# Kernel optimization log

Measured on AMD Instinct MI355X. Metric: run time of the kernel, lower is better.

Reference implementation:

```python
import jax, jax.numpy as jnp
import numpy as np

B, S, IN = 8, 1024, 64
D, F, H, L = 512, 2048, 8, 6
HD = D // H
EPS = 1e-5
GATE_TEMP = 1.0


def _rmsnorm(x, scale):
    return x * scale * jax.lax.rsqrt(jnp.mean(x * x, axis=-1, keepdims=True) + EPS)


def _sinusoidal_pe(seq_len, d_model):
    pos = np.arange(seq_len)[:, None].astype(np.float32)
    div = np.exp(np.arange(0, d_model, 2).astype(np.float32) * (-np.log(10000.0) / d_model))
    pe = np.zeros((seq_len, d_model), dtype=np.float32)
    pe[:, 0::2] = np.sin(pos * div)
    pe[:, 1::2] = np.cos(pos * div)
    return jnp.asarray(pe)


def setup_inputs() -> dict:
    key = jax.random.key(0)
    ks = jax.random.split(key, 12)
    s = 0.02
    return {
        "src": jax.random.normal(ks[0], (B, S, IN), jnp.float32),
        "in_w": jax.random.normal(ks[1], (IN, D), jnp.float32) * s,
        "in_b": jnp.zeros((D,), jnp.float32),
        "Wq": jax.random.normal(ks[2], (L, D, D), jnp.float32) * s,
        "Wk": jax.random.normal(ks[3], (L, D, D), jnp.float32) * s,
        "Wv": jax.random.normal(ks[4], (L, D, D), jnp.float32) * s,
        "Wo": jax.random.normal(ks[5], (L, D, D), jnp.float32) * s,
        "bq": jnp.zeros((L, D), jnp.float32),
        "bk": jnp.zeros((L, D), jnp.float32),
        "bv": jnp.zeros((L, D), jnp.float32),
        "bo": jnp.zeros((L, D), jnp.float32),
        "n1": jnp.ones((L, D), jnp.float32),
        "n2": jnp.ones((L, D), jnp.float32),
        "Wg": jax.random.normal(ks[6], (L, D, F), jnp.float32) * s,
        "Wu": jax.random.normal(ks[7], (L, D, F), jnp.float32) * s,
        "Wd": jax.random.normal(ks[8], (L, F, D), jnp.float32) * s,
        "gate_w": jax.random.normal(ks[9], (L, D), jnp.float32) * s,
        "gate_b": jnp.full((L,), 2.0, jnp.float32),  # LayerGate init_bias=2.0
        "final_scale": jnp.ones((D,), jnp.float32),
    }


def reference(src, in_w, in_b, Wq, Wk, Wv, Wo, bq, bk, bv, bo, n1, n2,
              Wg, Wu, Wd, gate_w, gate_b, final_scale):
    b, s, _ = src.shape
    x = src @ in_w + in_b                      # input_adapter: [B,S,D]
    x = x + _sinusoidal_pe(s, D)               # PositionalEncoding, scale=1.0
    inv_sqrt_hd = 1.0 / jnp.sqrt(jnp.asarray(HD, x.dtype))
    for i in range(L):
        # --- pre-norm self-attention block ---
        h = _rmsnorm(x, n1[i])
        q = (h @ Wq[i] + bq[i]).reshape(b, s, H, HD)
        k = (h @ Wk[i] + bk[i]).reshape(b, s, H, HD)
        v = (h @ Wv[i] + bv[i]).reshape(b, s, H, HD)
        scores = jnp.einsum("bqhd,bkhd->bhqk", q, k) * inv_sqrt_hd
        attn = jax.nn.softmax(scores, axis=-1)
        ctx = jnp.einsum("bhqk,bkhd->bqhd", attn, v).reshape(b, s, D)
        y = x + (ctx @ Wo[i] + bo[i])
        # --- pre-norm SwiGLU FFN block ---
        h2 = _rmsnorm(y, n2[i])
        y = y + (jax.nn.silu(h2 @ Wg[i]) * (h2 @ Wu[i])) @ Wd[i]
        # --- LayerGate: seq-mode hard skip with straight-through estimator ---
        pooled = jnp.mean(x, axis=1)                           # gate on layer input [B,D]
        p = jax.nn.sigmoid((pooled @ gate_w[i] + gate_b[i]) / GATE_TEMP)  # [B]
        hard = (p > 0.5).astype(x.dtype)
        g = hard + p - jax.lax.stop_gradient(p)
        x = g[:, None, None] * y + (1.0 - g)[:, None, None] * x
    return _rmsnorm(x, final_scale)
```

## Files before the change

### kernel.cpp

```cpp
#include <hip/hip_runtime.h>


typedef unsigned short u16;
typedef __attribute__((ext_vector_type(8))) __bf16 bf16x8;
typedef __attribute__((ext_vector_type(4))) float f32x4;
typedef __attribute__((ext_vector_type(16))) float f32x16;
typedef __attribute__((ext_vector_type(8))) unsigned short u16x8;

#define DEV __device__ __forceinline__

DEV u16 f2bf(float f) {
  unsigned u = __builtin_bit_cast(unsigned, f);
  u += 0x7fffu + ((u >> 16) & 1u);
  return (u16)(u >> 16);
}
DEV float bf2f(u16 h) { return __builtin_bit_cast(float, ((unsigned)h) << 16); }

DEV void gload16(const void* g, void* l) {
  __builtin_amdgcn_global_load_lds(
      (__attribute__((address_space(1))) void*)g,
      (__attribute__((address_space(3))) void*)l, 16, 0, 0);
}

DEV void xcd_map(int& bx, int& by) {
  const int nx = gridDim.x, ny = gridDim.y;
  const int orig = bx * ny + by;
  const int cpx = (nx * ny) >> 3;
  const int swz = (orig & 7) * cpx + (orig >> 3);
  bx = swz / ny; by = swz - bx * ny;
}

__global__ __launch_bounds__(256) void transpose_all_kernel(
    const float* __restrict__ Wq, const float* __restrict__ Wk,
    const float* __restrict__ Wv, const float* __restrict__ Wo,
    const float* __restrict__ Wg, const float* __restrict__ Wu,
    const float* __restrict__ Wd,
    u16* __restrict__ WqkvT, u16* __restrict__ WoT, u16* __restrict__ WgT,
    u16* __restrict__ WuT, u16* __restrict__ WdT)
{
  const int l = blockIdx.y;
  const int idx = blockIdx.x;
  const float* src; u16* dst; int N, bx, by;
  if (idx < 1024) {
    const int w = idx >> 8, t = idx & 255;
    bx = t & 15; by = t >> 4; N = 512;
    const size_t lo = (size_t)l * 262144;
    if (w == 0)      { src = Wq + lo; dst = WqkvT + (size_t)l * 786432; }
    else if (w == 1) { src = Wk + lo; dst = WqkvT + (size_t)l * 786432 + 262144; }
    else if (w == 2) { src = Wv + lo; dst = WqkvT + (size_t)l * 786432 + 524288; }
    else             { src = Wo + lo; dst = WoT + lo; }
  } else if (idx < 2048) {
    const int t = idx - 1024; bx = t & 63; by = t >> 6; N = 2048;
    src = Wg + (size_t)l * 1048576; dst = WgT + (size_t)l * 1048576;
  } else if (idx < 3072) {
    const int t = idx - 2048; bx = t & 63; by = t >> 6; N = 2048;
    src = Wu + (size_t)l * 1048576; dst = WuT + (size_t)l * 1048576;
  } else {
    const int t = idx - 3072; bx = t & 15; by = t >> 4; N = 512;
    src = Wd + (size_t)l * 1048576; dst = WdT + (size_t)l * 1048576;
  }
  const int K = (idx >= 3072) ? 2048 : 512;
  __shared__ float tl[32][33];
  const int n0 = bx * 32, k0 = by * 32;
  const int tx = threadIdx.x & 31, ty = threadIdx.x >> 5;
#pragma unroll
  for (int i = 0; i < 4; ++i)
    tl[ty + i * 8][tx] = src[(size_t)(k0 + ty + i * 8) * N + n0 + tx];
  __syncthreads();
#pragma unroll
  for (int i = 0; i < 4; ++i)
    dst[(size_t)(n0 + ty + i * 8) * K + k0 + tx] = f2bf(tl[tx][ty + i * 8]);
}

__global__ void biaspack_kernel(const float* __restrict__ bq,
                                const float* __restrict__ bk,
                                const float* __restrict__ bv,
                                float* __restrict__ out)
{
  const int l = blockIdx.x;
  for (int c = threadIdx.x; c < 1536; c += 256) {
    float v = (c < 512) ? bq[l * 512 + c]
            : (c < 1024) ? bk[l * 512 + c - 512]
                         : bv[l * 512 + c - 1024];
    out[l * 1536 + c] = v;
  }
}

__global__ __launch_bounds__(256) void adapter_kernel(
    const float* __restrict__ src, const float* __restrict__ w,
    const float* __restrict__ bias, float* __restrict__ x)
{
  __shared__ float srow[8][64];
  const int m0 = blockIdx.y * 8;
  const int n = blockIdx.x * 256 + threadIdx.x;
  for (int i = threadIdx.x; i < 512; i += 256)
    srow[i >> 6][i & 63] = src[(size_t)m0 * 64 + i];
  __syncthreads();
  float acc[8];
#pragma unroll
  for (int r = 0; r < 8; ++r) acc[r] = bias[n];
  for (int k = 0; k < 64; ++k) {
    const float wv = w[(size_t)k * 512 + n];
#pragma unroll
    for (int r = 0; r < 8; ++r) acc[r] = fmaf(srow[r][k], wv, acc[r]);
  }
  const int i2 = n & ~1;
  const float freq = expf((float)i2 * (-9.210340371976184f / 512.0f));
#pragma unroll
  for (int r = 0; r < 8; ++r) {
    const int pos = (m0 + r) & 1023;
    const float ang = (float)pos * freq;
    acc[r] += (n & 1) ? cosf(ang) : sinf(ang);
    x[(size_t)(m0 + r) * 512 + n] = acc[r];
  }
}

template <bool BF16OUT>
__global__ __launch_bounds__(256) void rmsnorm_kernel(
    const float* __restrict__ x, const float* __restrict__ scale,
    u16* __restrict__ outb, float* __restrict__ outf)
{
  const int wave = threadIdx.x >> 6, lane = threadIdx.x & 63;
  const size_t row = (size_t)blockIdx.x * 4 + wave;
  const f32x4* xr = (const f32x4*)(x + row * 512);
  f32x4 a = xr[lane * 2], c = xr[lane * 2 + 1];
  float ss = a[0]*a[0] + a[1]*a[1] + a[2]*a[2] + a[3]*a[3]
           + c[0]*c[0] + c[1]*c[1] + c[2]*c[2] + c[3]*c[3];
#pragma unroll
  for (int d = 1; d < 64; d <<= 1) ss += __shfl_xor(ss, d);
  const float r = rsqrtf(ss * (1.0f / 512.0f) + 1e-5f);
  const f32x4* sr = (const f32x4*)scale;
  f32x4 s1 = sr[lane * 2], s2 = sr[lane * 2 + 1];
  if (BF16OUT) {
    u16x8 ov;
    ov[0] = f2bf(a[0] * s1[0] * r); ov[1] = f2bf(a[1] * s1[1] * r);
    ov[2] = f2bf(a[2] * s1[2] * r); ov[3] = f2bf(a[3] * s1[3] * r);
    ov[4] = f2bf(c[0] * s2[0] * r); ov[5] = f2bf(c[1] * s2[1] * r);
    ov[6] = f2bf(c[2] * s2[2] * r); ov[7] = f2bf(c[3] * s2[3] * r);
    *(u16x8*)(outb + row * 512 + lane * 8) = ov;
  } else {
    f32x4 o1, o2;
    o1[0] = a[0]*s1[0]*r; o1[1] = a[1]*s1[1]*r; o1[2] = a[2]*s1[2]*r; o1[3] = a[3]*s1[3]*r;
    o2[0] = c[0]*s2[0]*r; o2[1] = c[1]*s2[1]*r; o2[2] = c[2]*s2[2]*r; o2[3] = c[3]*s2[3]*r;
    f32x4* orow = (f32x4*)(outf + row * 512);
    orow[lane * 2] = o1; orow[lane * 2 + 1] = o2;
  }
}

template <int MODE, int BN>
__global__ __launch_bounds__(256) void gemm_bt(
    const u16* __restrict__ A, const u16* __restrict__ Bt,
    const float* __restrict__ bias, const float* __restrict__ resf,
    float* __restrict__ outf, u16* __restrict__ outb,
    const float* __restrict__ gatep, int M, int N, int K)
{
  constexpr int NI = BN / 32;
  constexpr int BROUNDS = BN / 64;
  __shared__ __align__(16) u16 lA[128 * 32];
  __shared__ __align__(16) u16 lB[BN * 32];
  const int tid = threadIdx.x;
  const int wave = tid >> 6, lane = tid & 63;
  const int lr = lane & 15, lg = lane >> 4;
  int bx = blockIdx.x, by = blockIdx.y;
  xcd_map(bx, by);
  const int m0 = by << 7, n0 = bx * BN;
  const int wr = wave >> 1, wc = wave & 1;
  if (MODE == 4) {
    if (gatep[m0 >> 10] == 0.0f) return;
  }
  f32x4 acc[4][NI] = {};
  for (int kt = 0; kt < K; kt += 32) {
    __syncthreads();
#pragma unroll
    for (int i = 0; i < 2; ++i) {
      const int c = i * 256 + tid;
      const int row = c >> 2, kc = (c & 3) << 3;
      gload16(A + (size_t)(m0 + row) * K + kt + kc,
              lA + (size_t)(i * 256 + wave * 64) * 8);
    }
#pragma unroll
    for (int i = 0; i < BROUNDS; ++i) {
      const int c = i * 256 + tid;
      const int row = c >> 2, kc = (c & 3) << 3;
      gload16(Bt + (size_t)(n0 + row) * K + kt + kc,
              lB + (size_t)(i * 256 + wave * 64) * 8);
    }
    __syncthreads();
    bf16x8 af[4], bfr[NI];
#pragma unroll
    for (int mi = 0; mi < 4; ++mi)
      af[mi] = *(const bf16x8*)&lA[(wr * 64 + mi * 16 + lr) * 32 + lg * 8];
#pragma unroll
    for (int ni = 0; ni < NI; ++ni)
      bfr[ni] = *(const bf16x8*)&lB[(wc * (BN / 2) + ni * 16 + lr) * 32 + lg * 8];
#pragma unroll
    for (int mi = 0; mi < 4; ++mi)
#pragma unroll
      for (int ni = 0; ni < NI; ++ni)
        acc[mi][ni] = __builtin_amdgcn_mfma_f32_16x16x32_bf16(
            af[mi], bfr[ni], acc[mi][ni], 0, 0, 0);
  }
#pragma unroll
  for (int mi = 0; mi < 4; ++mi) {
#pragma unroll
    for (int ni = 0; ni < NI; ++ni) {
      const int col = n0 + wc * (BN / 2) + ni * 16 + lr;
      const float bs = (MODE == 0 || MODE == 1) ? bias[col] : 0.0f;
#pragma unroll
      for (int j = 0; j < 4; ++j) {
        const int row = m0 + wr * 64 + mi * 16 + lg * 4 + j;
        const size_t idx = (size_t)row * N + col;
        float v = acc[mi][ni][j] + bs;
        if (MODE == 0) {
          if (col < 512) v *= 0.125f;
          outb[idx] = f2bf(v);
        } else {
          outf[idx] = v + resf[idx];
        }
      }
    }
  }
}

__global__ __launch_bounds__(256) void gemm_glu(
    const u16* __restrict__ A, const u16* __restrict__ Bg,
    const u16* __restrict__ Bu, u16* __restrict__ outT)
{
  constexpr int K = 512, N = 2048;
  __shared__ __align__(16) u16 lA[128 * 32];
  __shared__ __align__(16) u16 lG[64 * 32];
  __shared__ __align__(16) u16 lU[64 * 32];
  const int tid = threadIdx.x;
  const int wave = tid >> 6, lane = tid & 63;
  const int lr = lane & 15, lg = lane >> 4;
  int bx = blockIdx.x, by = blockIdx.y;
  xcd_map(bx, by);
  const int m0 = by << 7, n0 = bx << 6;
  const int wr = wave >> 1, wc = wave & 1;
  f32x4 ag[4][2] = {}, au[4][2] = {};
  for (int kt = 0; kt < K; kt += 32) {
    __syncthreads();
#pragma unroll
    for (int i = 0; i < 2; ++i) {
      const int c = i * 256 + tid;
      const int row = c >> 2, kc = (c & 3) << 3;
      gload16(A + (size_t)(m0 + row) * K + kt + kc,
              lA + (size_t)(i * 256 + wave * 64) * 8);
    }
    {
      const int row = tid >> 2, kc = (tid & 3) << 3;
      gload16(Bg + (size_t)(n0 + row) * K + kt + kc, lG + (size_t)(wave * 64) * 8);
      gload16(Bu + (size_t)(n0 + row) * K + kt + kc, lU + (size_t)(wave * 64) * 8);
    }
    __syncthreads();
    bf16x8 af[4], gf[2], uf[2];
#pragma unroll
    for (int mi = 0; mi < 4; ++mi)
      af[mi] = *(const bf16x8*)&lA[(wr * 64 + mi * 16 + lr) * 32 + lg * 8];
#pragma unroll
    for (int ni = 0; ni < 2; ++ni) {
      gf[ni] = *(const bf16x8*)&lG[(wc * 32 + ni * 16 + lr) * 32 + lg * 8];
      uf[ni] = *(const bf16x8*)&lU[(wc * 32 + ni * 16 + lr) * 32 + lg * 8];
    }
#pragma unroll
    for (int mi = 0; mi < 4; ++mi)
#pragma unroll
      for (int ni = 0; ni < 2; ++ni) {
        ag[mi][ni] = __builtin_amdgcn_mfma_f32_16x16x32_bf16(
            af[mi], gf[ni], ag[mi][ni], 0, 0, 0);
        au[mi][ni] = __builtin_amdgcn_mfma_f32_16x16x32_bf16(
            af[mi], uf[ni], au[mi][ni], 0, 0, 0);
      }
  }
#pragma unroll
  for (int mi = 0; mi < 4; ++mi) {
#pragma unroll
    for (int ni = 0; ni < 2; ++ni) {
      const int col = n0 + wc * 32 + ni * 16 + lr;
#pragma unroll
      for (int j = 0; j < 4; ++j) {
        const int row = m0 + wr * 64 + mi * 16 + lg * 4 + j;
        const float g = ag[mi][ni][j];
        const float sg = g / (1.0f + __expf(-g));
        outT[(size_t)row * N + col] = f2bf(sg * au[mi][ni][j]);
      }
    }
  }
}

__global__ __launch_bounds__(256) void attn_kernel(
    const u16* __restrict__ qkv, u16* __restrict__ ctx)
{
  constexpr int LD = 1536;
  const int qblk = blockIdx.x, bh = blockIdx.y;
  const int b = bh >> 3, h = bh & 7;
  const int tid = threadIdx.x, wave = tid >> 6, lane = tid & 63;
  const int l31 = lane & 31, half = lane >> 5;
  const size_t rowb = (size_t)b * 1024;
  const int q0 = qblk * 128 + wave * 32;

  __shared__ __align__(16) u16 Ksh[2][64 * 64];
  __shared__ __align__(16) u16 Vsh[2][64 * 64];
  __shared__ __align__(16) u16 PL[4][32 * 64];
  __shared__ float rl_lds[4][32];

  const u16* qrow = qkv + (rowb + q0 + l31) * LD + h * 64;
  bf16x8 qf[4];
#pragma unroll
  for (int c = 0; c < 4; ++c)
    qf[c] = *(const bf16x8*)(qrow + c * 16 + half * 8);

  const int krow0 = tid >> 3;
  const int kch0 = (tid & 7) ^ (krow0 & 7);
  const int kch1 = (tid & 7) ^ ((krow0 + 32) & 7);
  const int vm = tid >> 3, vd0 = (tid & 7) * 8;
  const int vswz = (vm >> 2) ^ (tid & 7);
  char* vbase0 = (char*)Vsh + (vswz << 4) + ((vm & 3) << 2);
  const u16* kg = qkv + rowb * LD + 512 + h * 64;
  const u16* vg = qkv + (rowb + 2 * vm) * LD + 1024 + h * 64 + vd0;

  f32x16 o0 = {}, o1 = {};
  float l_acc = 0.0f;

  gload16(kg + (size_t)(0 + krow0) * LD + kch0 * 8, Ksh[0] + wave * 512);
  gload16(kg + (size_t)(32 + krow0) * LD + kch1 * 8, Ksh[0] + 2048 + wave * 512);
  {
    u16x8 va = *(const u16x8*)vg;
    u16x8 vb = *(const u16x8*)(vg + LD);
#pragma unroll
    for (int j = 0; j < 8; ++j) {
      const unsigned w = (unsigned)va[j] | ((unsigned)vb[j] << 16);
      *(unsigned*)(vbase0 + (vd0 + j) * 128) = w;
    }
  }
  __syncthreads();

  for (int t = 0; t < 16; ++t) {
    const int cur = t & 1, nxt = cur ^ 1;
    const int k0n = (t + 1) * 64;
    u16x8 va2, vb2;
    if (t < 15) {
      gload16(kg + (size_t)(k0n + krow0) * LD + kch0 * 8,
              Ksh[nxt] + wave * 512);
      gload16(kg + (size_t)(k0n + 32 + krow0) * LD + kch1 * 8,
              Ksh[nxt] + 2048 + wave * 512);
      va2 = *(const u16x8*)(vg + (size_t)k0n * LD);
      vb2 = *(const u16x8*)(vg + (size_t)k0n * LD + LD);
    }

    const char* kshb = (const char*)Ksh[cur];
    const char* vshb = (const char*)Vsh[cur];

    f32x16 s0 = {}, s1 = {};
#pragma unroll
    for (int c = 0; c < 4; ++c) {
      {
        const int row = l31;
        bf16x8 kf = *(const bf16x8*)(kshb + row * 128 +
                        ((((c << 1) | half) ^ (row & 7)) << 4));
        s0 = __builtin_amdgcn_mfma_f32_32x32x16_bf16(kf, qf[c], s0, 0, 0, 0);
      }
      {
        const int row = 32 + l31;
        bf16x8 kf = *(const bf16x8*)(kshb + row * 128 +
                        ((((c << 1) | half) ^ (row & 7)) << 4));
        s1 = __builtin_amdgcn_mfma_f32_32x32x16_bf16(kf, qf[c], s1, 0, 0, 0);
      }
    }

    char* plw = (char*)PL[wave];
#pragma unroll
    for (int blk = 0; blk < 2; ++blk) {
      const f32x16 sv = blk ? s1 : s0;
#pragma unroll
      for (int rg = 0; rg < 4; ++rg) {
        const float e0 = __expf(fminf(sv[rg * 4 + 0], 60.0f));
        const float e1 = __expf(fminf(sv[rg * 4 + 1], 60.0f));
        const float e2 = __expf(fminf(sv[rg * 4 + 2], 60.0f));
        const float e3 = __expf(fminf(sv[rg * 4 + 3], 60.0f));
        l_acc += (e0 + e1) + (e2 + e3);
        const unsigned lo = (unsigned)f2bf(e0) | ((unsigned)f2bf(e1) << 16);
        const unsigned hi = (unsigned)f2bf(e2) | ((unsigned)f2bf(e3) << 16);
        const int chunk = (rg + 4 * blk) ^ (l31 & 7);
        *(unsigned long long*)(plw + l31 * 128 + (chunk << 4) + half * 8) =
            (unsigned long long)lo | ((unsigned long long)hi << 32);
      }
    }

#pragma unroll
    for (int c = 0; c < 4; ++c) {
      bf16x8 pf = *(const bf16x8*)(plw + l31 * 128 +
                      ((((c << 1) | half) ^ (l31 & 7)) << 4));
      {
        const int row = l31;
        bf16x8 vf = *(const bf16x8*)(vshb + row * 128 +
                        ((((c << 1) | half) ^ (row >> 3)) << 4));
        o0 = __builtin_amdgcn_mfma_f32_32x32x16_bf16(pf, vf, o0, 0, 0, 0);
      }
      {
        const int row = 32 + l31;
        bf16x8 vf = *(const bf16x8*)(vshb + row * 128 +
                        ((((c << 1) | half) ^ (row >> 3)) << 4));
        o1 = __builtin_amdgcn_mfma_f32_32x32x16_bf16(pf, vf, o1, 0, 0, 0);
      }
    }

    if (t < 15) {
      char* vbn = (char*)Vsh[nxt] + (vswz << 4) + ((vm & 3) << 2);
#pragma unroll
      for (int j = 0; j < 8; ++j) {
        const unsigned w = (unsigned)va2[j] | ((unsigned)vb2[j] << 16);
        *(unsigned*)(vbn + (vd0 + j) * 128) = w;
      }
    }
    __syncthreads();
  }

  const float l_tot = l_acc + __shfl_xor(l_acc, 32);
  if (lane < 32) rl_lds[wave][l31] = 1.0f / l_tot;
  __syncthreads();
#pragma unroll
  for (int r = 0; r < 16; ++r) {
    const int q_r = (r & 3) + 8 * (r >> 2) + 4 * half;
    const float rl = rl_lds[wave][q_r];
    const size_t orow = (rowb + q0 + q_r) * 512 + h * 64 + l31;
    ctx[orow] = f2bf(o0[r] * rl);
    ctx[orow + 32] = f2bf(o1[r] * rl);
  }
}

__global__ __launch_bounds__(256) void gate_partial_kernel(
    const float* __restrict__ x, const float* __restrict__ gw,
    float* __restrict__ gp)
{
  const int b = blockIdx.x, chunk = blockIdx.y, tid = threadIdx.x;
  const float* xb = x + (size_t)b * 1024 * 512 + (size_t)chunk * 16 * 512;
  float acc = 0.0f;
#pragma unroll
  for (int k = 0; k < 8; ++k) {
    const int i = tid * 4 + k * 1024;
    f32x4 v = *(const f32x4*)(xb + i);
    f32x4 wv = *(const f32x4*)(gw + (i & 511));
    acc += v[0]*wv[0] + v[1]*wv[1] + v[2]*wv[2] + v[3]*wv[3];
  }
  __shared__ float red[256];
  red[tid] = acc;
  __syncthreads();
  for (int s = 128; s > 32; s >>= 1) {
    if (tid < s) red[tid] += red[tid + s];
    __syncthreads();
  }
  if (tid < 32) {
    float v = red[tid] + red[tid + 32];
#pragma unroll
    for (int d = 1; d < 32; d <<= 1) v += __shfl_xor(v, d);
    if (tid == 0) gp[b * 64 + chunk] = v;
  }
}

__global__ __launch_bounds__(512) void gate_final_kernel(
    const float* __restrict__ gp, const float* __restrict__ gb, int layer,
    float* __restrict__ gout)
{
  const int tid = threadIdx.x, b = tid >> 6, lane = tid & 63;
  float v = gp[tid];
#pragma unroll
  for (int d = 1; d < 64; d <<= 1) v += __shfl_xor(v, d);
  if (lane == 0) {
    const float val = v / 1024.0f + gb[layer];
    const float p = 1.0f / (1.0f + __expf(-val));
    gout[b] = (p > 0.5f) ? 1.0f : 0.0f;
  }
}

extern "C" void kernel_launch(void* const* d_in, const int* in_sizes, int n_in,
                              void* d_out, int out_size, void* d_ws, size_t ws_size,
                              hipStream_t stream)
{
  (void)in_sizes; (void)n_in; (void)out_size; (void)ws_size;
  const float* src  = (const float*)d_in[0];
  const float* in_w = (const float*)d_in[1];
  const float* in_b = (const float*)d_in[2];
  const float* Wq   = (const float*)d_in[3];
  const float* Wk   = (const float*)d_in[4];
  const float* Wv   = (const float*)d_in[5];
  const float* Wo   = (const float*)d_in[6];
  const float* bq   = (const float*)d_in[7];
  const float* bk   = (const float*)d_in[8];
  const float* bv   = (const float*)d_in[9];
  const float* bo   = (const float*)d_in[10];
  const float* n1   = (const float*)d_in[11];
  const float* n2   = (const float*)d_in[12];
  const float* Wg   = (const float*)d_in[13];
  const float* Wu   = (const float*)d_in[14];
  const float* Wd   = (const float*)d_in[15];
  const float* gw   = (const float*)d_in[16];
  const float* gb   = (const float*)d_in[17];
  const float* fs   = (const float*)d_in[18];

  char* ws = (char*)d_ws;
  size_t off = 0;
  auto alloc = [&](size_t bytes) -> void* {
    void* p = ws + off;
    off += (bytes + 255) & ~(size_t)255;
    return p;
  };
  u16*   WqkvT = (u16*)alloc(6ULL * 1536 * 512 * 2);
  u16*   WoT   = (u16*)alloc(6ULL * 512 * 512 * 2);
  u16*   WgT   = (u16*)alloc(6ULL * 2048 * 512 * 2);
  u16*   WuT   = (u16*)alloc(6ULL * 2048 * 512 * 2);
  u16*   WdT   = (u16*)alloc(6ULL * 512 * 2048 * 2);
  float* bqkv  = (float*)alloc(6ULL * 1536 * 4);
  float* x     = (float*)alloc(8192ULL * 512 * 4);
  float* y     = (float*)alloc(8192ULL * 512 * 4);
  u16*   hbuf  = (u16*)alloc(8192ULL * 512 * 2);
  u16*   sA    = (u16*)alloc(8192ULL * 2048 * 2);
  u16*   sB    = (u16*)alloc(8192ULL * 2048 * 2);
  float* gp    = (float*)alloc(512 * 4);
  float* gate  = (float*)alloc(64 * 4);

  const dim3 tb(256);
  transpose_all_kernel<<<dim3(4096, 6), tb, 0, stream>>>(
      Wq, Wk, Wv, Wo, Wg, Wu, Wd, WqkvT, WoT, WgT, WuT, WdT);
  biaspack_kernel<<<6, tb, 0, stream>>>(bq, bk, bv, bqkv);
  adapter_kernel<<<dim3(2, 1024), tb, 0, stream>>>(src, in_w, in_b, x);

  for (int l = 0; l < 6; ++l) {
    gate_partial_kernel<<<dim3(8, 64), tb, 0, stream>>>(x, gw + l * 512, gp);
    gate_final_kernel<<<1, 512, 0, stream>>>(gp, gb, l, gate);
    rmsnorm_kernel<true><<<2048, tb, 0, stream>>>(x, n1 + l * 512, hbuf, nullptr);
    gemm_bt<0, 128><<<dim3(12, 64), tb, 0, stream>>>(
        hbuf, WqkvT + (size_t)l * 1536 * 512, bqkv + l * 1536,
        nullptr, nullptr, sA, nullptr, 8192, 1536, 512);
    attn_kernel<<<dim3(8, 64), tb, 0, stream>>>(sA, sB);
    gemm_bt<1, 64><<<dim3(8, 64), tb, 0, stream>>>(
        sB, WoT + (size_t)l * 512 * 512, bo + l * 512,
        x, y, nullptr, nullptr, 8192, 512, 512);
    rmsnorm_kernel<true><<<2048, tb, 0, stream>>>(y, n2 + l * 512, hbuf, nullptr);
    gemm_glu<<<dim3(32, 64), tb, 0, stream>>>(
        hbuf, WgT + (size_t)l * 2048 * 512, WuT + (size_t)l * 2048 * 512, sB);
    gemm_bt<4, 64><<<dim3(8, 64), tb, 0, stream>>>(
        sB, WdT + (size_t)l * 512 * 2048, nullptr,
        y, x, nullptr, gate, 8192, 512, 2048);
  }
  rmsnorm_kernel<false><<<2048, tb, 0, stream>>>(x, fs, nullptr, (float*)d_out);
}
```

Baseline: 1.128 ms.

## Double GEMM K-tile with XOR-swizzled LDS, fold gate final into down GEMM

The GEMM kernels now stage 64-wide K tiles instead of 32, with an XOR swizzle on the LDS layout. This halves the barrier and loop iterations and should cut LDS bank conflicts. The separate gate_final launch is removed, and each down-projection block reduces the gate partials itself and compares against zero instead of applying a sigmoid. The XCD block mapping switches to row-major order, and the attention kernel's second K-chunk swizzle index is simplified. LDS use per block roughly doubles, which may lower occupancy.

```diff
diff --git a/kernel.cpp b/kernel.cpp
--- a/kernel.cpp
+++ b/kernel.cpp
@@ -24,10 +24,10 @@
 
 DEV void xcd_map(int& bx, int& by) {
   const int nx = gridDim.x, ny = gridDim.y;
-  const int orig = bx * ny + by;
+  const int orig = by * nx + bx;
   const int cpx = (nx * ny) >> 3;
   const int swz = (orig & 7) * cpx + (orig >> 3);
-  bx = swz / ny; by = swz - bx * ny;
+  by = swz / nx; bx = swz - by * nx;
 }
 
 __global__ __launch_bounds__(256) void transpose_all_kernel(
@@ -152,12 +152,12 @@
     const u16* __restrict__ A, const u16* __restrict__ Bt,
     const float* __restrict__ bias, const float* __restrict__ resf,
     float* __restrict__ outf, u16* __restrict__ outb,
-    const float* __restrict__ gatep, int M, int N, int K)
+    const float* __restrict__ gatep, const float* __restrict__ gbias,
+    int layer, int M, int N, int K)
 {
   constexpr int NI = BN / 32;
-  constexpr int BROUNDS = BN / 64;
-  __shared__ __align__(16) u16 lA[128 * 32];
-  __shared__ __align__(16) u16 lB[BN * 32];
+  __shared__ __align__(16) u16 lA[128 * 64];
+  __shared__ __align__(16) u16 lB[BN * 64];
   const int tid = threadIdx.x;
   const int wave = tid >> 6, lane = tid & 63;
   const int lr = lane & 15, lg = lane >> 4;
@@ -166,39 +166,56 @@
   const int m0 = by << 7, n0 = bx * BN;
   const int wr = wave >> 1, wc = wave & 1;
   if (MODE == 4) {
-    if (gatep[m0 >> 10] == 0.0f) return;
+    __shared__ float gfl;
+    if (tid < 64) {
+      float v = gatep[(m0 >> 10) * 64 + tid];
+#pragma unroll
+      for (int d = 1; d < 64; d <<= 1) v += __shfl_xor(v, d);
+      if (tid == 0) gfl = (v / 1024.0f + gbias[layer] > 0.0f) ? 1.0f : 0.0f;
+    }
+    __syncthreads();
+    if (gfl == 0.0f) return;
   }
   f32x4 acc[4][NI] = {};
-  for (int kt = 0; kt < K; kt += 32) {
-    __syncthreads();
-#pragma unroll
-    for (int i = 0; i < 2; ++i) {
+  for (int kt = 0; kt < K; kt += 64) {
+    __syncthreads();
+#pragma unroll
+    for (int i = 0; i < 4; ++i) {
       const int c = i * 256 + tid;
-      const int row = c >> 2, kc = (c & 3) << 3;
+      const int row = c >> 3, kc = ((c & 7) ^ (row & 7)) << 3;
       gload16(A + (size_t)(m0 + row) * K + kt + kc,
               lA + (size_t)(i * 256 + wave * 64) * 8);
     }
 #pragma unroll
-    for (int i = 0; i < BROUNDS; ++i) {
+    for (int i = 0; i < BN / 32; ++i) {
       const int c = i * 256 + tid;
-      const int row = c >> 2, kc = (c & 3) << 3;
+      const int row = c >> 3, kc = ((c & 7) ^ (row & 7)) << 3;
       gload16(Bt + (size_t)(n0 + row) * K + kt + kc,
               lB + (size_t)(i * 256 + wave * 64) * 8);
     }
     __syncthreads();
-    bf16x8 af[4], bfr[NI];
-#pragma unroll
-    for (int mi = 0; mi < 4; ++mi)
-      af[mi] = *(const bf16x8*)&lA[(wr * 64 + mi * 16 + lr) * 32 + lg * 8];
-#pragma unroll
-    for (int ni = 0; ni < NI; ++ni)
-      bfr[ni] = *(const bf16x8*)&lB[(wc * (BN / 2) + ni * 16 + lr) * 32 + lg * 8];
-#pragma unroll
-    for (int mi = 0; mi < 4; ++mi)
-#pragma unroll
-      for (int ni = 0; ni < NI; ++ni)
-        acc[mi][ni] = __builtin_amdgcn_mfma_f32_16x16x32_bf16(
-            af[mi], bfr[ni], acc[mi][ni], 0, 0, 0);
+    bf16x8 af[2][4], bfr[2][NI];
+#pragma unroll
+    for (int kk = 0; kk < 2; ++kk) {
+#pragma unroll
+      for (int mi = 0; mi < 4; ++mi) {
+        const int row = wr * 64 + mi * 16 + lr;
+        af[kk][mi] = *(const bf16x8*)&lA[row * 64 + (((kk * 4 + lg) ^ (row & 7)) << 3)];
+      }
+#pragma unroll
+      for (int ni = 0; ni < NI; ++ni) {
+        const int row = wc * (BN / 2) + ni * 16 + lr;
+        bfr[kk][ni] = *(const bf16x8*)&lB[row * 64 + (((kk * 4 + lg) ^ (row & 7)) << 3)];
+      }
+    }
+#pragma unroll
+    for (int kk = 0; kk < 2; ++kk)
+#pragma unroll
+      for (int mi = 0; mi < 4; ++mi)
+#pragma unroll
+        for (int ni = 0; ni < NI; ++ni)
+          acc[mi][ni] = __builtin_amdgcn_mfma_f32_16x16x32_bf16(
+              af[kk][mi], bfr[kk][ni], acc[mi][ni], 0, 0, 0);
   }
 #pragma unroll
   for (int mi = 0; mi < 4; ++mi) {
@@ -227,9 +244,9 @@
     const u16* __restrict__ Bu, u16* __restrict__ outT)
 {
   constexpr int K = 512, N = 2048;
-  __shared__ __align__(16) u16 lA[128 * 32];
-  __shared__ __align__(16) u16 lG[64 * 32];
-  __shared__ __align__(16) u16 lU[64 * 32];
+  __shared__ __align__(16) u16 lA[128 * 64];
+  __shared__ __align__(16) u16 lG[64 * 64];
+  __shared__ __align__(16) u16 lU[64 * 64];
   const int tid = threadIdx.x;
   const int wave = tid >> 6, lane = tid & 63;
   const int lr = lane & 15, lg = lane >> 4;
@@ -238,39 +255,51 @@
   const int m0 = by << 7, n0 = bx << 6;
   const int wr = wave >> 1, wc = wave & 1;
   f32x4 ag[4][2] = {}, au[4][2] = {};
-  for (int kt = 0; kt < K; kt += 32) {
-    __syncthreads();
+  for (int kt = 0; kt < K; kt += 64) {
+    __syncthreads();
+#pragma unroll
+    for (int i = 0; i < 4; ++i) {
+      const int c = i * 256 + tid;
+      const int row = c >> 3, kc = ((c & 7) ^ (row & 7)) << 3;
+      gload16(A + (size_t)(m0 + row) * K + kt + kc,
+              lA + (size_t)(i * 256 + wave * 64) * 8);
+    }
 #pragma unroll
     for (int i = 0; i < 2; ++i) {
       const int c = i * 256 + tid;
-      const int row = c >> 2, kc = (c & 3) << 3;
-      gload16(A + (size_t)(m0 + row) * K + kt + kc,
-              lA + (size_t)(i * 256 + wave * 64) * 8);
-    }
-    {
-      const int row = tid >> 2, kc = (tid & 3) << 3;
-      gload16(Bg + (size_t)(n0 + row) * K + kt + kc, lG + (size_t)(wave * 64) * 8);
-      gload16(Bu + (size_t)(n0 + row) * K + kt + kc, lU + (size_t)(wave * 64) * 8);
-    }
-    __syncthreads();
-    bf16x8 af[4], gf[2], uf[2];
-#pragma unroll
-    for (int mi = 0; mi < 4; ++mi)
-      af[mi] = *(const bf16x8*)&lA[(wr * 64 + mi * 16 + lr) * 32 + lg * 8];
-#pragma unroll
-    for (int ni = 0; ni < 2; ++ni) {
-      gf[ni] = *(const bf16x8*)&lG[(wc * 32 + ni * 16 + lr) * 32 + lg * 8];
-      uf[ni] = *(const bf16x8*)&lU[(wc * 32 + ni * 16 + lr) * 32 + lg * 8];
-    }
-#pragma unroll
-    for (int mi = 0; mi < 4; ++mi)
+      const int row = c >> 3, kc = ((c & 7) ^ (row & 7)) << 3;
+      const size_t dst = (size_t)(i * 256 + wave * 64) * 8;
+      gload16(Bg + (size_t)(n0 + row) * K + kt + kc, lG + dst);
+      gload16(Bu + (size_t)(n0 + row) * K + kt + kc, lU + dst);
+    }
+    __syncthreads();
+    bf16x8 af[2][4], gf[2][2], uf[2][2];
+#pragma unroll
+    for (int kk = 0; kk < 2; ++kk) {
+#pragma unroll
+      for (int mi = 0; mi < 4; ++mi) {
+        const int row = wr * 64 + mi * 16 + lr;
+        af[kk][mi] = *(const bf16x8*)&lA[row * 64 + (((kk * 4 + lg) ^ (row & 7)) << 3)];
+      }
 #pragma unroll
       for (int ni = 0; ni < 2; ++ni) {
-        ag[mi][ni] = __builtin_amdgcn_mfma_f32_16x16x32_bf16(
-            af[mi], gf[ni], ag[mi][ni], 0, 0, 0);
-        au[mi][ni] = __builtin_amdgcn_mfma_f32_16x16x32_bf16(
-            af[mi], uf[ni], au[mi][ni], 0, 0, 0);
-      }
+        const int row = wc * 32 + ni * 16 + lr;
+        const int off = row * 64 + (((kk * 4 + lg) ^ (row & 7)) << 3);
+        gf[kk][ni] = *(const bf16x8*)&lG[off];
+        uf[kk][ni] = *(const bf16x8*)&lU[off];
+      }
+    }
+#pragma unroll
+    for (int kk = 0; kk < 2; ++kk)
+#pragma unroll
+      for (int mi = 0; mi < 4; ++mi)
+#pragma unroll
+        for (int ni = 0; ni < 2; ++ni) {
+          ag[mi][ni] = __builtin_amdgcn_mfma_f32_16x16x32_bf16(
+              af[kk][mi], gf[kk][ni], ag[mi][ni], 0, 0, 0);
+          au[mi][ni] = __builtin_amdgcn_mfma_f32_16x16x32_bf16(
+              af[kk][mi], uf[kk][ni], au[mi][ni], 0, 0, 0);
+        }
   }
 #pragma unroll
   for (int mi = 0; mi < 4; ++mi) {
@@ -312,7 +341,6 @@
 
   const int krow0 = tid >> 3;
   const int kch0 = (tid & 7) ^ (krow0 & 7);
-  const int kch1 = (tid & 7) ^ ((krow0 + 32) & 7);
   const int vm = tid >> 3, vd0 = (tid & 7) * 8;
   const int vswz = (vm >> 2) ^ (tid & 7);
   char* vbase0 = (char*)Vsh + (vswz << 4) + ((vm & 3) << 2);
@@ -323,7 +351,7 @@
   float l_acc = 0.0f;
 
   gload16(kg + (size_t)(0 + krow0) * LD + kch0 * 8, Ksh[0] + wave * 512);
-  gload16(kg + (size_t)(32 + krow0) * LD + kch1 * 8, Ksh[0] + 2048 + wave * 512);
+  gload16(kg + (size_t)(32 + krow0) * LD + kch0 * 8, Ksh[0] + 2048 + wave * 512);
   {
     u16x8 va = *(const u16x8*)vg;
     u16x8 vb = *(const u16x8*)(vg + LD);
@@ -342,7 +370,7 @@
     if (t < 15) {
       gload16(kg + (size_t)(k0n + krow0) * LD + kch0 * 8,
               Ksh[nxt] + wave * 512);
-      gload16(kg + (size_t)(k0n + 32 + krow0) * LD + kch1 * 8,
+      gload16(kg + (size_t)(k0n + 32 + krow0) * LD + kch0 * 8,
               Ksh[nxt] + 2048 + wave * 512);
       va2 = *(const u16x8*)(vg + (size_t)k0n * LD);
       vb2 = *(const u16x8*)(vg + (size_t)k0n * LD + LD);
@@ -455,21 +483,6 @@
 #pragma unroll
     for (int d = 1; d < 32; d <<= 1) v += __shfl_xor(v, d);
     if (tid == 0) gp[b * 64 + chunk] = v;
-  }
-}
-
-__global__ __launch_bounds__(512) void gate_final_kernel(
-    const float* __restrict__ gp, const float* __restrict__ gb, int layer,
-    float* __restrict__ gout)
-{
-  const int tid = threadIdx.x, b = tid >> 6, lane = tid & 63;
-  float v = gp[tid];
-#pragma unroll
-  for (int d = 1; d < 64; d <<= 1) v += __shfl_xor(v, d);
-  if (lane == 0) {
-    const float val = v / 1024.0f + gb[layer];
-    const float p = 1.0f / (1.0f + __expf(-val));
-    gout[b] = (p > 0.5f) ? 1.0f : 0.0f;
   }
 }
 
@@ -517,7 +530,6 @@
   u16*   sA    = (u16*)alloc(8192ULL * 2048 * 2);
   u16*   sB    = (u16*)alloc(8192ULL * 2048 * 2);
   float* gp    = (float*)alloc(512 * 4);
-  float* gate  = (float*)alloc(64 * 4);
 
   const dim3 tb(256);
   transpose_all_kernel<<<dim3(4096, 6), tb, 0, stream>>>(
@@ -527,21 +539,20 @@
 
   for (int l = 0; l < 6; ++l) {
     gate_partial_kernel<<<dim3(8, 64), tb, 0, stream>>>(x, gw + l * 512, gp);
-    gate_final_kernel<<<1, 512, 0, stream>>>(gp, gb, l, gate);
     rmsnorm_kernel<true><<<2048, tb, 0, stream>>>(x, n1 + l * 512, hbuf, nullptr);
     gemm_bt<0, 128><<<dim3(12, 64), tb, 0, stream>>>(
         hbuf, WqkvT + (size_t)l * 1536 * 512, bqkv + l * 1536,
-        nullptr, nullptr, sA, nullptr, 8192, 1536, 512);
+        nullptr, nullptr, sA, nullptr, nullptr, 0, 8192, 1536, 512);
     attn_kernel<<<dim3(8, 64), tb, 0, stream>>>(sA, sB);
     gemm_bt<1, 64><<<dim3(8, 64), tb, 0, stream>>>(
         sB, WoT + (size_t)l * 512 * 512, bo + l * 512,
-        x, y, nullptr, nullptr, 8192, 512, 512);
+        x, y, nullptr, nullptr, nullptr, 0, 8192, 512, 512);
     rmsnorm_kernel<true><<<2048, tb, 0, stream>>>(y, n2 + l * 512, hbuf, nullptr);
     gemm_glu<<<dim3(32, 64), tb, 0, stream>>>(
         hbuf, WgT + (size_t)l * 2048 * 512, WuT + (size_t)l * 2048 * 512, sB);
     gemm_bt<4, 64><<<dim3(8, 64), tb, 0, stream>>>(
         sB, WdT + (size_t)l * 512 * 2048, nullptr,
-        y, x, nullptr, gate, 8192, 512, 2048);
+        y, x, nullptr, gp, gb, l, 8192, 512, 2048);
   }
   rmsnorm_kernel<false><<<2048, tb, 0, stream>>>(x, fs, nullptr, (float*)d_out);
 }
```

Measured after the change: 1.015 ms. 1.11x faster.
